# Optimization experiments

Hardware: AMD Instinct MI355X
Metric: run time of the kernel (lower is better)

The kernel has to match this reference:

```python
import jax, jax.numpy as jnp
import numpy as np

D_GNN, D_MODEL = 512, 2048
B, T = 4, 4096
EPS = 1e-5


def layer_norm(x, gamma, beta):
    mu = jnp.mean(x, axis=-1, keepdims=True)
    var = jnp.mean(jnp.square(x - mu), axis=-1, keepdims=True)
    return (x - mu) * jax.lax.rsqrt(var + EPS) * gamma + beta


def setup_inputs() -> dict:
    key = jax.random.key(0)
    ks = jax.random.split(key, 10)
    s_proj = 1.0 / np.sqrt(D_GNN)
    s_mod = 1.0 / np.sqrt(D_MODEL)
    s_gate = 1.0 / np.sqrt(2 * D_MODEL)
    return {
        "h_llm": jax.random.normal(ks[0], (B, T, D_MODEL), jnp.float32),
        "h_change": jax.random.normal(ks[1], (B, D_GNN), jnp.float32),
        # h_change_proj: Linear(d_gnn -> d_model)
        "w_proj": jax.random.uniform(ks[2], (D_MODEL, D_GNN), jnp.float32, -s_proj, s_proj),
        "b_proj": jnp.zeros((D_MODEL,), jnp.float32),
        "g1": jnp.ones((D_MODEL,), jnp.float32),
        "b1": jnp.zeros((D_MODEL,), jnp.float32),
        # MHA value / output projections (q,k are mathematically irrelevant: kv_len==1 -> softmax==1)
        "w_v": jax.random.uniform(ks[3], (D_MODEL, D_MODEL), jnp.float32, -s_mod, s_mod),
        "b_v": jnp.zeros((D_MODEL,), jnp.float32),
        "w_o": jax.random.uniform(ks[4], (D_MODEL, D_MODEL), jnp.float32, -s_mod, s_mod),
        "b_o": jnp.zeros((D_MODEL,), jnp.float32),
        "g2": jnp.ones((D_MODEL,), jnp.float32),
        "b2": jnp.zeros((D_MODEL,), jnp.float32),
        # fusion gate: Linear(2*d_model -> d_model) + sigmoid
        "w_gate": jax.random.uniform(ks[5], (D_MODEL, 2 * D_MODEL), jnp.float32, -s_gate, s_gate),
        "b_gate": jnp.zeros((D_MODEL,), jnp.float32),
        "g3": jnp.ones((D_MODEL,), jnp.float32),
        "b3": jnp.zeros((D_MODEL,), jnp.float32),
    }


def reference(h_llm, h_change, w_proj, b_proj, g1, b1, w_v, b_v, w_o, b_o,
              g2, b2, w_gate, b_gate, g3, b3):
    # project GNN feature to d_model, then LayerNorm  -> (B, D)
    hc = layer_norm(h_change @ w_proj.T + b_proj, g1, b1)
    # cross-attention with kv_len == 1: softmax over a single key is identically 1,
    # so attn_output == out_proj(value_proj(hc)), broadcast over T. Dropout is eval (identity).
    attn = (hc @ w_v.T + b_v) @ w_o.T + b_o                 # (B, D)
    attn_out = layer_norm(h_llm + attn[:, None, :], g2, b2)  # (B, T, D)
    # gated residual fusion: gate = sigmoid(W [h_llm ; attn_out] + b)
    wg_l, wg_a = w_gate[:, :D_MODEL], w_gate[:, D_MODEL:]
    gate = jax.nn.sigmoid(h_llm @ wg_l.T + attn_out @ wg_a.T + b_gate)
    fused = gate * attn_out + (1.0 - gate) * h_llm
    return layer_norm(fused, g3, b3)
```

## Files before the change

### kernel.cpp

```cpp
#include <hip/hip_runtime.h>
#include <hip/hip_bf16.h>
#include <cstdint>
#include <cstddef>

#define DM 2048
#define DG 512
#define NBATCH 4
#define NT 4096
#define NM (NBATCH*NT)
#define KC (2*DM)
#define LN_EPS 1e-5f
#define NTILES (KC/128)
#define SCL_A 16.0f
#define SCL_B 8192.0f
#define DESCALE (1.0f/131072.0f)
#define INV_SCL_A 0.0625f

typedef __bf16 bf16;
typedef bf16 bf16x8 __attribute__((ext_vector_type(8)));
typedef float f32x4 __attribute__((ext_vector_type(4)));
typedef int   i32x4 __attribute__((ext_vector_type(4)));
typedef char  i8x8  __attribute__((ext_vector_type(8)));
typedef unsigned char u8x8 __attribute__((ext_vector_type(8)));

#define AS1 __attribute__((address_space(1)))
#define AS3 __attribute__((address_space(3)))

__device__ __forceinline__ char q8(float x, float s) {
    int v = (int)rintf(x * s);
    v = v > 127 ? 127 : (v < -127 ? -127 : v);
    return (char)v;
}

__device__ __forceinline__ void block_reduce_2(float& s, float& s2) {
#pragma unroll
    for (int off = 32; off; off >>= 1) {
        s  += __shfl_down(s, off);
        s2 += __shfl_down(s2, off);
    }
    __shared__ float sm[8];
    const int wid = threadIdx.x >> 6, lane = threadIdx.x & 63;
    if (lane == 0) { sm[wid] = s; sm[4 + wid] = s2; }
    __syncthreads();
    s  = sm[0] + sm[1] + sm[2] + sm[3];
    s2 = sm[4] + sm[5] + sm[6] + sm[7];
}

__global__ void k_pack_dot1(const float* __restrict__ wg, int8_t* __restrict__ wqb,
                            const float* __restrict__ X, const float* __restrict__ W,
                            const float* __restrict__ bias, float* __restrict__ out) {
    if (blockIdx.x >= 512) {
        const int i = (blockIdx.x - 512) * 256 + threadIdx.x;
        const f32x4* s = (const f32x4*)wg + (size_t)i * 2;
        f32x4 a = s[0], b = s[1];
        i8x8 o;
#pragma unroll
        for (int q = 0; q < 4; q++) { o[q] = q8(a[q], SCL_B); o[4+q] = q8(b[q], SCL_B); }
        *((i8x8*)wqb + i) = o;
        return;
    }
    const int lane = threadIdx.x & 63;
    const int wid  = threadIdx.x >> 6;
    const int j = blockIdx.x * 4 + wid;
    const f32x4* Wr = (const f32x4*)(W + (size_t)j * DG);
    float acc[NBATCH] = {0.f, 0.f, 0.f, 0.f};
    constexpr int C = DG / 4 / 64;
#pragma unroll
    for (int i = 0; i < C; i++) {
        f32x4 wv = Wr[lane + 64 * i];
#pragma unroll
        for (int b = 0; b < NBATCH; b++) {
            f32x4 xv = ((const f32x4*)(X + (size_t)b * DG))[lane + 64 * i];
            acc[b] += wv[0]*xv[0] + wv[1]*xv[1] + wv[2]*xv[2] + wv[3]*xv[3];
        }
    }
#pragma unroll
    for (int off = 32; off; off >>= 1)
#pragma unroll
        for (int b = 0; b < NBATCH; b++) acc[b] += __shfl_down(acc[b], off);
    if (lane == 0) {
        const float bb = bias[j];
#pragma unroll
        for (int b = 0; b < NBATCH; b++) out[(size_t)b * DM + j] = acc[b] + bb;
    }
}

template<int K>
__global__ void k_dot(const float* __restrict__ X, const float* __restrict__ W,
                      const float* __restrict__ bias, float* __restrict__ out) {
    const int lane = threadIdx.x & 63;
    const int wid  = threadIdx.x >> 6;
    const int j = blockIdx.x * 4 + wid;
    const f32x4* Wr = (const f32x4*)(W + (size_t)j * K);
    float acc[NBATCH] = {0.f, 0.f, 0.f, 0.f};
    constexpr int C = K / 4 / 64;
#pragma unroll
    for (int i = 0; i < C; i++) {
        f32x4 wv = Wr[lane + 64 * i];
#pragma unroll
        for (int b = 0; b < NBATCH; b++) {
            f32x4 xv = ((const f32x4*)(X + (size_t)b * K))[lane + 64 * i];
            acc[b] += wv[0]*xv[0] + wv[1]*xv[1] + wv[2]*xv[2] + wv[3]*xv[3];
        }
    }
#pragma unroll
    for (int off = 32; off; off >>= 1)
#pragma unroll
        for (int b = 0; b < NBATCH; b++) acc[b] += __shfl_down(acc[b], off);
    if (lane == 0) {
        const float bb = bias[j];
#pragma unroll
        for (int b = 0; b < NBATCH; b++) out[(size_t)b * DM + j] = acc[b] + bb;
    }
}

__global__ void k_ln_small(const float* __restrict__ in, const float* __restrict__ g,
                           const float* __restrict__ bt, float* __restrict__ out) {
    const int row = blockIdx.x;
    const int tid = threadIdx.x;
    const f32x4* ir = (const f32x4*)(in + (size_t)row * DM);
    f32x4 v0 = ir[tid], v1 = ir[tid + 256];
    float s  = v0[0]+v0[1]+v0[2]+v0[3] + v1[0]+v1[1]+v1[2]+v1[3];
    float s2 = v0[0]*v0[0]+v0[1]*v0[1]+v0[2]*v0[2]+v0[3]*v0[3]
             + v1[0]*v1[0]+v1[1]*v1[1]+v1[2]*v1[2]+v1[3]*v1[3];
    block_reduce_2(s, s2);
    const float mu = s * (1.0f / DM);
    const float r  = rsqrtf(s2 * (1.0f / DM) - mu * mu + LN_EPS);
    f32x4 g0 = ((const f32x4*)g)[tid],  g1v = ((const f32x4*)g)[tid + 256];
    f32x4 b0 = ((const f32x4*)bt)[tid], b1v = ((const f32x4*)bt)[tid + 256];
    f32x4 o0 = (v0 - mu) * r * g0 + b0;
    f32x4 o1 = (v1 - mu) * r * g1v + b1v;
    f32x4* orow = (f32x4*)(out + (size_t)row * DM);
    orow[tid] = o0; orow[tid + 256] = o1;
}

__global__ void k_stats_pack(const float* __restrict__ h, const float* __restrict__ attnv,
                             const float* __restrict__ g2, const float* __restrict__ b2,
                             int8_t* __restrict__ Aq,
                             float* __restrict__ muA, float* __restrict__ rA) {
    const int m = blockIdx.x;
    const int b = m >> 12;
    const int tid = threadIdx.x;
    const f32x4* hr = (const f32x4*)(h + (size_t)m * DM);
    const f32x4* ar = (const f32x4*)(attnv + (size_t)b * DM);
    f32x4 h0 = hr[2*tid], h1 = hr[2*tid + 1];
    f32x4 a0 = ar[2*tid], a1 = ar[2*tid + 1];
    f32x4 x0 = h0 + a0, x1 = h1 + a1;
    float s  = x0[0]+x0[1]+x0[2]+x0[3] + x1[0]+x1[1]+x1[2]+x1[3];
    float s2 = x0[0]*x0[0]+x0[1]*x0[1]+x0[2]*x0[2]+x0[3]*x0[3]
             + x1[0]*x1[0]+x1[1]*x1[1]+x1[2]*x1[2]+x1[3]*x1[3];
    block_reduce_2(s, s2);
    const float mu = s * (1.0f / DM);
    const float r  = rsqrtf(s2 * (1.0f / DM) - mu * mu + LN_EPS);
    if (tid == 0) { muA[m] = mu; rA[m] = r; }
    f32x4 gg0 = ((const f32x4*)g2)[2*tid], gg1 = ((const f32x4*)g2)[2*tid + 1];
    f32x4 bb0 = ((const f32x4*)b2)[2*tid], bb1 = ((const f32x4*)b2)[2*tid + 1];
    f32x4 ao0 = (x0 - mu) * r * gg0 + bb0;
    f32x4 ao1 = (x1 - mu) * r * gg1 + bb1;
    i8x8 qh, qa;
#pragma unroll
    for (int q = 0; q < 4; q++) {
        qh[q] = q8(h0[q], SCL_A);  qh[4+q] = q8(h1[q], SCL_A);
        qa[q] = q8(ao0[q], SCL_A); qa[4+q] = q8(ao1[q], SCL_A);
    }
    *(i8x8*)(Aq + (size_t)m * KC + 8*tid) = qh;
    *(i8x8*)(Aq + (size_t)m * KC + DM + 8*tid) = qa;
}

#define MF(a,b,c) __builtin_amdgcn_mfma_i32_16x16x64_i8(a,b,c,0,0,0)
#define SCHED0() __builtin_amdgcn_sched_barrier(0)
#define BAR()  { SCHED0(); asm volatile("s_barrier" ::: "memory"); SCHED0(); }
#define VM(n)  { asm volatile("s_waitcnt vmcnt(" #n ")" ::: "memory"); SCHED0(); }
#define LGKM(n) { asm volatile("s_waitcnt lgkmcnt(" #n ")" ::: "memory"); SCHED0(); }

__global__ __launch_bounds__(512, 2) void k_gemm256(const int8_t* __restrict__ A, const int8_t* __restrict__ Bw,
                                                    const float* __restrict__ bgate, uint8_t* __restrict__ gq) {
    __shared__ __align__(128) char smem[131072];
    const int tid  = threadIdx.x;
    const int lane = tid & 63;
    const int wid  = tid >> 6;
    const int wm   = wid >> 2, wn = wid & 3;

    const int swz = (blockIdx.x & 7) * 64 + (blockIdx.x >> 3);
    const int bm = (swz >> 3) << 8;
    const int bn = (swz & 7) << 8;

    const int r_local = tid >> 3;
    const int sc = (tid & 7) ^ (r_local & 7);
    const int8_t* Abase = A  + (size_t)(bm + r_local) * KC + sc*16;
    const int8_t* Bbase = Bw + (size_t)(bn + r_local) * KC + sc*16;
    const int ldsW = wid << 10;

#define STAGEA(buf, rnd, kt) __builtin_amdgcn_global_load_lds( \
        (const AS1 void*)(Abase + (size_t)(rnd)*64*KC + (kt)*128), \
        (AS3 void*)(smem + (buf)*65536 + (rnd)*8192 + ldsW), 16, 0, 0)
#define STAGEB(buf, rnd, kt) __builtin_amdgcn_global_load_lds( \
        (const AS1 void*)(Bbase + (size_t)(rnd)*64*KC + (kt)*128), \
        (AS3 void*)(smem + (buf)*65536 + 32768 + (rnd)*8192 + ldsW), 16, 0, 0)

    const int co0 = ((lane >> 4) ^ (lane & 7)) << 4;
    const int co1 = ((4 + (lane >> 4)) ^ (lane & 7)) << 4;
    const int arowb = (wm*128 + (lane & 15)) * 128;
    const int browb = (wn*64  + (lane & 15)) * 128;

#define AFRG(buf, m, ks) (*(const i32x4*)(smem + (buf)*65536 + arowb + (m)*2048 + ((ks) ? co1 : co0)))
#define BFRG(buf, n, ks) (*(const i32x4*)(smem + (buf)*65536 + 32768 + browb + (n)*2048 + ((ks) ? co1 : co0)))

    i32x4 acc[8][4] = {};
    i32x4 aLo[4][2], aHi[4][2], b01[2][2], b23[2][2];

#define LOAD_ALO(buf) { _Pragma("unroll") for (int i = 0; i < 4; i++) { aLo[i][0] = AFRG(buf,i,0);   aLo[i][1] = AFRG(buf,i,1);   } }
#define LOAD_AHI(buf) { _Pragma("unroll") for (int i = 0; i < 4; i++) { aHi[i][0] = AFRG(buf,4+i,0); aHi[i][1] = AFRG(buf,4+i,1); } }
#define LOAD_B01(buf) { _Pragma("unroll") for (int j = 0; j < 2; j++) { b01[j][0] = BFRG(buf,j,0);   b01[j][1] = BFRG(buf,j,1);   } }
#define LOAD_B23(buf) { _Pragma("unroll") for (int j = 0; j < 2; j++) { b23[j][0] = BFRG(buf,2+j,0); b23[j][1] = BFRG(buf,2+j,1); } }

#define MMQ(MOFF, AF, BF, NOFF) { _Pragma("unroll") for (int i = 0; i < 4; i++) \
        _Pragma("unroll") for (int j = 0; j < 2; j++) { \
            acc[(MOFF)+i][(NOFF)+j] = MF(AF[i][0], BF[j][0], acc[(MOFF)+i][(NOFF)+j]); \
            acc[(MOFF)+i][(NOFF)+j] = MF(AF[i][1], BF[j][1], acc[(MOFF)+i][(NOFF)+j]); } }

    STAGEB(0,0,0); STAGEB(0,1,0); STAGEB(0,2,0); STAGEB(0,3,0);
    STAGEA(0,0,0); STAGEA(0,2,0); STAGEA(0,1,0); STAGEA(0,3,0);
    VM(0);
    BAR();

#define TILE_BODY(TT, BUF, NBUF) { \
    const bool g = (TT) < NTILES - 1; \
     \
    if (g) { STAGEB(NBUF,0,(TT)+1); STAGEB(NBUF,1,(TT)+1); STAGEB(NBUF,2,(TT)+1); STAGEB(NBUF,3,(TT)+1); } \
    LOAD_ALO(BUF); LOAD_B01(BUF); LOAD_B23(BUF); SCHED0(); \
    LGKM(4); \
    __builtin_amdgcn_s_setprio(1); \
    MMQ(0, aLo, b01, 0); \
    __builtin_amdgcn_s_setprio(0); SCHED0(); \
     \
    if (g) { STAGEA(NBUF,0,(TT)+1); STAGEA(NBUF,1,(TT)+1); STAGEA(NBUF,2,(TT)+1); STAGEA(NBUF,3,(TT)+1); } \
    LOAD_AHI(BUF); SCHED0(); \
    LGKM(8); \
    __builtin_amdgcn_s_setprio(1); \
    MMQ(0, aLo, b23, 2); \
    __builtin_amdgcn_s_setprio(0); SCHED0(); \
     \
    LGKM(0); \
    __builtin_amdgcn_s_setprio(1); \
    MMQ(4, aHi, b23, 2); \
    __builtin_amdgcn_s_setprio(0); SCHED0(); \
     \
    __builtin_amdgcn_s_setprio(1); \
    MMQ(4, aHi, b01, 0); \
    __builtin_amdgcn_s_setprio(0); SCHED0(); \
    VM(0); \
    BAR(); \
}

    for (int T = 0; T < NTILES; T += 2) {
        TILE_BODY(T,   0, 1);
        TILE_BODY(T+1, 1, 0);
    }

#pragma unroll
    for (int n = 0; n < 4; n++) {
        const int col = bn + wn*64 + n*16 + (lane & 15);
        const float bg = bgate[col];
#pragma unroll
        for (int m = 0; m < 8; m++) {
            const int row = bm + wm*128 + m*16 + ((lane >> 4) << 2);
#pragma unroll
            for (int r = 0; r < 4; r++) {
                const float z = (float)acc[m][n][r] * DESCALE + bg;
                const float gate = 1.0f / (1.0f + __expf(-z));
                gq[(size_t)(row + r) * DM + col] = (uint8_t)(int)rintf(gate * 255.0f);
            }
        }
    }
}

__global__ void k_epilogue(const int8_t* __restrict__ Aq, const uint8_t* __restrict__ gq,
                           const float* __restrict__ attnv, const float* __restrict__ muA,
                           const float* __restrict__ rA,
                           const float* __restrict__ g2, const float* __restrict__ b2,
                           const float* __restrict__ g3, const float* __restrict__ b3,
                           float* __restrict__ out) {
    const int m = blockIdx.x;
    const int b = m >> 12;
    const int tid = threadIdx.x;
    i8x8 qh = *(const i8x8*)(Aq + (size_t)m * KC + 8*tid);
    f32x4 h0, h1;
#pragma unroll
    for (int q = 0; q < 4; q++) { h0[q] = (float)qh[q] * INV_SCL_A; h1[q] = (float)qh[4+q] * INV_SCL_A; }
    const f32x4* ar = (const f32x4*)(attnv + (size_t)b * DM);
    f32x4 a0 = ar[2*tid], a1 = ar[2*tid + 1];
    const float mu = muA[m];
    const float r  = rA[m];
    f32x4 gg0 = ((const f32x4*)g2)[2*tid], gg1 = ((const f32x4*)g2)[2*tid + 1];
    f32x4 bb0 = ((const f32x4*)b2)[2*tid], bb1 = ((const f32x4*)b2)[2*tid + 1];
    f32x4 ao0 = (h0 + a0 - mu) * r * gg0 + bb0;
    f32x4 ao1 = (h1 + a1 - mu) * r * gg1 + bb1;
    u8x8 qv = *(const u8x8*)(gq + (size_t)m * DM + 8*tid);
    f32x4 gt0, gt1;
#pragma unroll
    for (int q = 0; q < 4; q++) {
        gt0[q] = (float)qv[q]   * (1.0f / 255.0f);
        gt1[q] = (float)qv[4+q] * (1.0f / 255.0f);
    }
    f32x4 f0 = h0 + gt0 * (ao0 - h0);
    f32x4 f1 = h1 + gt1 * (ao1 - h1);
    float s  = f0[0]+f0[1]+f0[2]+f0[3] + f1[0]+f1[1]+f1[2]+f1[3];
    float s2 = f0[0]*f0[0]+f0[1]*f0[1]+f0[2]*f0[2]+f0[3]*f0[3]
             + f1[0]*f1[0]+f1[1]*f1[1]+f1[2]*f1[2]+f1[3]*f1[3];
    block_reduce_2(s, s2);
    const float mu3 = s * (1.0f / DM);
    const float r3  = rsqrtf(s2 * (1.0f / DM) - mu3 * mu3 + LN_EPS);
    f32x4 g30 = ((const f32x4*)g3)[2*tid], g31 = ((const f32x4*)g3)[2*tid + 1];
    f32x4 b30 = ((const f32x4*)b3)[2*tid], b31 = ((const f32x4*)b3)[2*tid + 1];
    f32x4 o0 = (f0 - mu3) * r3 * g30 + b30;
    f32x4 o1 = (f1 - mu3) * r3 * g31 + b31;
    f32x4* orow = (f32x4*)(out + (size_t)m * DM);
    orow[2*tid] = o0; orow[2*tid + 1] = o1;
}

extern "C" void kernel_launch(void* const* d_in, const int* in_sizes, int n_in,
                              void* d_out, int out_size, void* d_ws, size_t ws_size,
                              hipStream_t stream) {
    const float* h_llm    = (const float*)d_in[0];
    const float* h_change = (const float*)d_in[1];
    const float* w_proj   = (const float*)d_in[2];
    const float* b_proj   = (const float*)d_in[3];
    const float* g1       = (const float*)d_in[4];
    const float* b1       = (const float*)d_in[5];
    const float* w_v      = (const float*)d_in[6];
    const float* b_v      = (const float*)d_in[7];
    const float* w_o      = (const float*)d_in[8];
    const float* b_o      = (const float*)d_in[9];
    const float* g2       = (const float*)d_in[10];
    const float* b2       = (const float*)d_in[11];
    const float* w_gate   = (const float*)d_in[12];
    const float* b_gate   = (const float*)d_in[13];
    const float* g3       = (const float*)d_in[14];
    const float* b3       = (const float*)d_in[15];
    float* out = (float*)d_out;

    char* ws = (char*)d_ws;
    int8_t* Aq  = (int8_t*)ws; ws += (size_t)NM * KC;
    int8_t* wqb = (int8_t*)ws; ws += (size_t)DM * KC;
    uint8_t* gq = (uint8_t*)ws; ws += (size_t)NM * DM;
    float* muA = (float*)ws;  ws += (size_t)NM * 4;
    float* rA  = (float*)ws;  ws += (size_t)NM * 4;
    float* raw1 = (float*)ws; ws += (size_t)NBATCH * DM * 4;
    float* hc   = (float*)ws; ws += (size_t)NBATCH * DM * 4;
    float* raw2 = (float*)ws; ws += (size_t)NBATCH * DM * 4;
    float* attnv= (float*)ws; ws += (size_t)NBATCH * DM * 4;

    k_pack_dot1<<<4608, 256, 0, stream>>>(w_gate, wqb, h_change, w_proj, b_proj, raw1);
    k_ln_small<<<NBATCH, 256, 0, stream>>>(raw1, g1, b1, hc);
    k_dot<DM><<<DM / 4, 256, 0, stream>>>(hc, w_v, b_v, raw2);
    k_dot<DM><<<DM / 4, 256, 0, stream>>>(raw2, w_o, b_o, attnv);
    k_stats_pack<<<NM, 256, 0, stream>>>(h_llm, attnv, g2, b2, Aq, muA, rA);
    k_gemm256<<<512, 512, 0, stream>>>(Aq, wqb, b_gate, gq);
    k_epilogue<<<NM, 256, 0, stream>>>(Aq, gq, attnv, muA, rA, g2, b2, g3, b3, out);
}
```

Before: 236.7 us.

## Switch int8 gate GEMM to 64-wide K tiles with triple-buffered LDS pipeline

Restructures the int8 gate GEMM main loop to use K-tiles of 64 bytes instead of 128, with three rotating LDS buffers and prefetch two tiles ahead. LDS reads of A and B fragments are software-pipelined one row-block ahead of the MFMAs, and B fragments for the next tile are loaded during the current one. The aim is better overlap of global-to-LDS copies and LDS reads with MFMA work and lower LDS usage. In exchange there are twice as many barriers per K, more live registers, and a hand-tuned waitcnt schedule that is fragile.

Measured after the change: 252.1 us. 6.5% more time.

```diff
diff --git a/kernel.cpp b/kernel.cpp
--- a/kernel.cpp
+++ b/kernel.cpp
@@ -10,7 +10,7 @@
 #define NM (NBATCH*NT)
 #define KC (2*DM)
 #define LN_EPS 1e-5f
-#define NTILES (KC/128)
+#define NTILES (KC/64)
 #define SCL_A 16.0f
 #define SCL_B 8192.0f
 #define DESCALE (1.0f/131072.0f)
@@ -175,7 +175,7 @@
 
 __global__ __launch_bounds__(512, 2) void k_gemm256(const int8_t* __restrict__ A, const int8_t* __restrict__ Bw,
                                                     const float* __restrict__ bgate, uint8_t* __restrict__ gq) {
-    __shared__ __align__(128) char smem[131072];
+    __shared__ __align__(128) char smem[98304];
     const int tid  = threadIdx.x;
     const int lane = tid & 63;
     const int wid  = tid >> 6;
@@ -185,78 +185,86 @@
     const int bm = (swz >> 3) << 8;
     const int bn = (swz & 7) << 8;
 
-    const int r_local = tid >> 3;
-    const int sc = (tid & 7) ^ (r_local & 7);
+    const int r_local = tid >> 2;
+    const int sc = (tid & 3) ^ (r_local & 3);
     const int8_t* Abase = A  + (size_t)(bm + r_local) * KC + sc*16;
     const int8_t* Bbase = Bw + (size_t)(bn + r_local) * KC + sc*16;
     const int ldsW = wid << 10;
 
-#define STAGEA(buf, rnd, kt) __builtin_amdgcn_global_load_lds( \
-        (const AS1 void*)(Abase + (size_t)(rnd)*64*KC + (kt)*128), \
-        (AS3 void*)(smem + (buf)*65536 + (rnd)*8192 + ldsW), 16, 0, 0)
-#define STAGEB(buf, rnd, kt) __builtin_amdgcn_global_load_lds( \
-        (const AS1 void*)(Bbase + (size_t)(rnd)*64*KC + (kt)*128), \
-        (AS3 void*)(smem + (buf)*65536 + 32768 + (rnd)*8192 + ldsW), 16, 0, 0)
-
-    const int co0 = ((lane >> 4) ^ (lane & 7)) << 4;
-    const int co1 = ((4 + (lane >> 4)) ^ (lane & 7)) << 4;
-    const int arowb = (wm*128 + (lane & 15)) * 128;
-    const int browb = (wn*64  + (lane & 15)) * 128;
-
-#define AFRG(buf, m, ks) (*(const i32x4*)(smem + (buf)*65536 + arowb + (m)*2048 + ((ks) ? co1 : co0)))
-#define BFRG(buf, n, ks) (*(const i32x4*)(smem + (buf)*65536 + 32768 + browb + (n)*2048 + ((ks) ? co1 : co0)))
+#define STAGEAU(O, u, kt) __builtin_amdgcn_global_load_lds( \
+        (const AS1 void*)(Abase + (size_t)(u)*128*KC + (kt)*64), \
+        (AS3 void*)(smem + (O) + (u)*8192 + ldsW), 16, 0, 0)
+#define STAGEBU(O, u, kt) __builtin_amdgcn_global_load_lds( \
+        (const AS1 void*)(Bbase + (size_t)(u)*128*KC + (kt)*64), \
+        (AS3 void*)(smem + (O) + 16384 + (u)*8192 + ldsW), 16, 0, 0)
+
+    const int co   = ((lane >> 4) ^ (lane & 3)) << 4;
+    const int aoff = (wm*128 + (lane & 15)) * 64 + co;
+    const int boff = 16384 + (wn*64 + (lane & 15)) * 64 + co;
+
+#define DSA(O, m) (*(const i32x4*)(smem + (O) + aoff + (m)*1024))
+#define DSB(O, n) (*(const i32x4*)(smem + (O) + boff + (n)*1024))
 
     i32x4 acc[8][4] = {};
-    i32x4 aLo[4][2], aHi[4][2], b01[2][2], b23[2][2];
-
-#define LOAD_ALO(buf) { _Pragma("unroll") for (int i = 0; i < 4; i++) { aLo[i][0] = AFRG(buf,i,0);   aLo[i][1] = AFRG(buf,i,1);   } }
-#define LOAD_AHI(buf) { _Pragma("unroll") for (int i = 0; i < 4; i++) { aHi[i][0] = AFRG(buf,4+i,0); aHi[i][1] = AFRG(buf,4+i,1); } }
-#define LOAD_B01(buf) { _Pragma("unroll") for (int j = 0; j < 2; j++) { b01[j][0] = BFRG(buf,j,0);   b01[j][1] = BFRG(buf,j,1);   } }
-#define LOAD_B23(buf) { _Pragma("unroll") for (int j = 0; j < 2; j++) { b23[j][0] = BFRG(buf,2+j,0); b23[j][1] = BFRG(buf,2+j,1); } }
-
-#define MMQ(MOFF, AF, BF, NOFF) { _Pragma("unroll") for (int i = 0; i < 4; i++) \
-        _Pragma("unroll") for (int j = 0; j < 2; j++) { \
-            acc[(MOFF)+i][(NOFF)+j] = MF(AF[i][0], BF[j][0], acc[(MOFF)+i][(NOFF)+j]); \
-            acc[(MOFF)+i][(NOFF)+j] = MF(AF[i][1], BF[j][1], acc[(MOFF)+i][(NOFF)+j]); } }
-
-    STAGEB(0,0,0); STAGEB(0,1,0); STAGEB(0,2,0); STAGEB(0,3,0);
-    STAGEA(0,0,0); STAGEA(0,2,0); STAGEA(0,1,0); STAGEA(0,3,0);
+    i32x4 a0,a1,a2,a3,a4,a5,a6,a7;
+    i32x4 bc0,bc1,bc2,bc3, bn0,bn1,bn2,bn3;
+
+#define MM4(AR, B0,B1,B2,B3, M) { \
+    __builtin_amdgcn_s_setprio(1); \
+    acc[M][0] = MF(AR, B0, acc[M][0]); \
+    acc[M][1] = MF(AR, B1, acc[M][1]); \
+    acc[M][2] = MF(AR, B2, acc[M][2]); \
+    acc[M][3] = MF(AR, B3, acc[M][3]); \
+    __builtin_amdgcn_s_setprio(0); SCHED0(); }
+
+#define TFULL(T_, O0_, O1_, O2_, C0,C1,C2,C3, N0,N1,N2,N3, G2_) { \
+    if (G2_) { STAGEAU(O0_ ,0,0); }  }
+
+#undef TFULL
+#define TFULL(T_, O0_, O1_, O2_, C0,C1,C2,C3, N0,N1,N2,N3, G2_) { \
+    if (G2_) { STAGEAU(O2_, 0, (T_)+2); } \
+    a2 = DSA(O0_, 2); SCHED0(); LGKM(2); MM4(a0, C0,C1,C2,C3, 0); \
+    if (G2_) { STAGEAU(O2_, 1, (T_)+2); } \
+    a3 = DSA(O0_, 3); SCHED0(); LGKM(2); MM4(a1, C0,C1,C2,C3, 1); \
+    if (G2_) { STAGEBU(O2_, 0, (T_)+2); } \
+    a4 = DSA(O0_, 4); N0 = DSB(O1_, 0); SCHED0(); LGKM(3); MM4(a2, C0,C1,C2,C3, 2); \
+    if (G2_) { STAGEBU(O2_, 1, (T_)+2); } \
+    a5 = DSA(O0_, 5); N1 = DSB(O1_, 1); SCHED0(); LGKM(4); MM4(a3, C0,C1,C2,C3, 3); \
+    a6 = DSA(O0_, 6); N2 = DSB(O1_, 2); SCHED0(); LGKM(5); MM4(a4, C0,C1,C2,C3, 4); \
+    a7 = DSA(O0_, 7); N3 = DSB(O1_, 3); SCHED0(); LGKM(5); MM4(a5, C0,C1,C2,C3, 5); \
+    a0 = DSA(O1_, 0); SCHED0(); LGKM(4); MM4(a6, C0,C1,C2,C3, 6); \
+    a1 = DSA(O1_, 1); SCHED0(); LGKM(3); MM4(a7, C0,C1,C2,C3, 7); \
+    VM(0); \
+    BAR(); }
+
+#define TTAIL(O0_, C0,C1,C2,C3) { \
+    a2 = DSA(O0_, 2); SCHED0(); LGKM(2); MM4(a0, C0,C1,C2,C3, 0); \
+    a3 = DSA(O0_, 3); SCHED0(); LGKM(2); MM4(a1, C0,C1,C2,C3, 1); \
+    a4 = DSA(O0_, 4); SCHED0(); LGKM(2); MM4(a2, C0,C1,C2,C3, 2); \
+    a5 = DSA(O0_, 5); SCHED0(); LGKM(2); MM4(a3, C0,C1,C2,C3, 3); \
+    a6 = DSA(O0_, 6); SCHED0(); LGKM(2); MM4(a4, C0,C1,C2,C3, 4); \
+    a7 = DSA(O0_, 7); SCHED0(); LGKM(2); MM4(a5, C0,C1,C2,C3, 5); \
+    LGKM(1); MM4(a6, C0,C1,C2,C3, 6); \
+    LGKM(0); MM4(a7, C0,C1,C2,C3, 7); }
+
+#define ROT() { int t_ = o0; o0 = o1; o1 = o2; o2 = t_; }
+
+    int o0 = 0, o1 = 32768, o2 = 65536;
+
+    STAGEAU(0, 0, 0); STAGEAU(0, 1, 0); STAGEBU(0, 0, 0); STAGEBU(0, 1, 0);
+    STAGEAU(32768, 0, 1); STAGEAU(32768, 1, 1); STAGEBU(32768, 0, 1); STAGEBU(32768, 1, 1);
     VM(0);
     BAR();
-
-#define TILE_BODY(TT, BUF, NBUF) { \
-    const bool g = (TT) < NTILES - 1; \
-     \
-    if (g) { STAGEB(NBUF,0,(TT)+1); STAGEB(NBUF,1,(TT)+1); STAGEB(NBUF,2,(TT)+1); STAGEB(NBUF,3,(TT)+1); } \
-    LOAD_ALO(BUF); LOAD_B01(BUF); LOAD_B23(BUF); SCHED0(); \
-    LGKM(4); \
-    __builtin_amdgcn_s_setprio(1); \
-    MMQ(0, aLo, b01, 0); \
-    __builtin_amdgcn_s_setprio(0); SCHED0(); \
-     \
-    if (g) { STAGEA(NBUF,0,(TT)+1); STAGEA(NBUF,1,(TT)+1); STAGEA(NBUF,2,(TT)+1); STAGEA(NBUF,3,(TT)+1); } \
-    LOAD_AHI(BUF); SCHED0(); \
-    LGKM(8); \
-    __builtin_amdgcn_s_setprio(1); \
-    MMQ(0, aLo, b23, 2); \
-    __builtin_amdgcn_s_setprio(0); SCHED0(); \
-     \
-    LGKM(0); \
-    __builtin_amdgcn_s_setprio(1); \
-    MMQ(4, aHi, b23, 2); \
-    __builtin_amdgcn_s_setprio(0); SCHED0(); \
-     \
-    __builtin_amdgcn_s_setprio(1); \
-    MMQ(4, aHi, b01, 0); \
-    __builtin_amdgcn_s_setprio(0); SCHED0(); \
-    VM(0); \
-    BAR(); \
-}
-
-    for (int T = 0; T < NTILES; T += 2) {
-        TILE_BODY(T,   0, 1);
-        TILE_BODY(T+1, 1, 0);
-    }
+    bc0 = DSB(0, 0); bc1 = DSB(0, 1); bc2 = DSB(0, 2); bc3 = DSB(0, 3);
+    a0 = DSA(0, 0); a1 = DSA(0, 1); SCHED0();
+
+    for (int it = 0; it < 31; ++it) {
+        const int T = 2 * it;
+        TFULL(T,   o0, o1, o2, bc0,bc1,bc2,bc3, bn0,bn1,bn2,bn3, true); ROT();
+        TFULL(T+1, o0, o1, o2, bn0,bn1,bn2,bn3, bc0,bc1,bc2,bc3, true); ROT();
+    }
+    TFULL(62, o0, o1, o2, bc0,bc1,bc2,bc3, bn0,bn1,bn2,bn3, false); ROT();
+    TTAIL(o0, bn0,bn1,bn2,bn3);
 
 #pragma unroll
     for (int n = 0; n < 4; n++) {
```
